# Kernel optimization log

Hardware: AMD Instinct MI355X
Metric: run time of the kernel (lower is better)

## Reference

```python
import jax, jax.numpy as jnp
import numpy as np
import math

DIM_PER_HEAD = 64

def setup_inputs() -> dict:
    key = jax.random.key(0)
    k1, k2, k3, k4 = jax.random.split(key, 4)
    B, H, S, D = 2, 16, 2048, 64
    mat1 = jax.random.normal(k1, (B, H, S, D), dtype=jnp.float32)
    mat2 = jax.random.normal(k2, (B, H, S, D), dtype=jnp.float32)
    mat3 = jax.random.normal(k3, (B, H, S, D), dtype=jnp.float32)
    bias = jax.random.normal(k4, (1, 1, S, S), dtype=jnp.float32)
    return {"mat1": mat1, "mat2": mat2, "mat3": mat3, "bias": bias}

def reference(mat1, mat2, mat3, bias) -> jnp.ndarray:
    # scale Q, scores = QK^T + bias, softmax over last dim, then @ V
    scale = 1.0 / math.sqrt(DIM_PER_HEAD)
    qk = jnp.einsum('bhqd,bhkd->bhqk', mat1 * scale, mat2)  # [B,H,S,S]
    scores = jax.nn.softmax(qk + bias, axis=-1)
    return jnp.einsum('bhqk,bhkd->bhqd', scores, mat3)
```

## Files before the change

### kernel.cpp

```cpp
#include <hip/hip_runtime.h>
#include <hip/hip_bf16.h>


#define SEQ 2048
#define DH  64
#define BHN 32
#define LOG2E 1.44269504088896f

typedef __attribute__((ext_vector_type(8))) short bf16x8;
typedef __attribute__((ext_vector_type(4))) float f32x4;
typedef __attribute__((ext_vector_type(8))) short short8v;

__device__ inline short f2b(float x) {
    union { float f; unsigned u; } v; v.f = x;
    unsigned r = v.u + 0x7fff + ((v.u >> 16) & 1);
    return (short)(r >> 16);
}

__device__ inline void gl_lds16(const void* g, void* l) {
    __builtin_amdgcn_global_load_lds(
        (const __attribute__((address_space(1))) void*)g,
        (__attribute__((address_space(3))) void*)l, 16, 0, 0);
}

__global__ __launch_bounds__(256)
void prep_kv(const float* __restrict__ K, const float* __restrict__ V,
             short* __restrict__ Kb, short* __restrict__ Vt) {
    __shared__ short t[64 * 72];
    const int tid = threadIdx.x;
    const int bh = blockIdx.x >> 5, st = blockIdx.x & 31, s0 = st * 64;

    {
        const float* Kp = K + ((size_t)bh * SEQ + s0) * DH;
        short* Ko = Kb + ((size_t)bh * SEQ + s0) * DH;
        #pragma unroll
        for (int i = 0; i < 2; ++i) {
            size_t o = (size_t)(tid + i * 256) * 8;
            f32x4 a = *(const f32x4*)(Kp + o);
            f32x4 b = *(const f32x4*)(Kp + o + 4);
            short8v s;
            #pragma unroll
            for (int j = 0; j < 4; ++j) { s[j] = f2b(a[j]); s[4 + j] = f2b(b[j]); }
            *(short8v*)(Ko + o) = s;
        }
    }

    const float* Vb = V + (size_t)bh * SEQ * DH + (size_t)s0 * DH;
    #pragma unroll
    for (int i = 0; i < 4; ++i) {
        int c = tid + i * 256, s = c >> 4, c4 = c & 15;
        f32x4 v = *(const f32x4*)(Vb + s * DH + c4 * 4);
        #pragma unroll
        for (int j = 0; j < 4; ++j) t[s * 72 + c4 * 4 + j] = f2b(v[j]);
    }
    __syncthreads();
    const int d = tid >> 2, part = tid & 3;
    short8v lo, hi;
    #pragma unroll
    for (int j = 0; j < 8; ++j) {
        lo[j] = t[(part * 16 + j) * 72 + d];
        hi[j] = t[(part * 16 + 8 + j) * 72 + d];
    }
    short* outp = Vt + (size_t)bh * DH * SEQ + (size_t)d * SEQ + s0 + part * 16;
    *(short8v*)outp = lo;
    *(short8v*)(outp + 8) = hi;
}

__global__ __launch_bounds__(256, 4)
void mha_main(const float* __restrict__ Q, const float* __restrict__ Bias,
              const short* __restrict__ Kb, const short* __restrict__ Vt,
              float* __restrict__ Out)
{
    __shared__ short ka[64 * DH];
    __shared__ short kbuf[64 * DH];
    __shared__ short va[64 * DH];
    __shared__ short vbuf[64 * DH];
    __shared__ short lds_p[4 * 16 * 64];

    const int tid = threadIdx.x, lane = tid & 63, wave = tid >> 6;
    const int l15 = lane & 15, l4 = lane >> 4;
    const int qb = blockIdx.x & 31, bh = blockIdx.x >> 5;
    const int q0 = qb * 64;

    const float* Qb = Q + (size_t)bh * SEQ * DH;
    const short* Kh = Kb + (size_t)bh * SEQ * DH;
    const short* Vh = Vt + (size_t)bh * DH * SEQ;
    float* Ob = Out + (size_t)bh * SEQ * DH;

    bf16x8 qf[2];
    {
        const float* qp = Qb + (size_t)(q0 + wave * 16 + l15) * DH;
        #pragma unroll
        for (int ks = 0; ks < 2; ++ks) {
            short tmp[8];
            #pragma unroll
            for (int j = 0; j < 8; ++j) tmp[j] = f2b(qp[ks * 32 + l4 * 8 + j] * 0.125f);
            qf[ks] = *reinterpret_cast<bf16x8*>(tmp);
        }
    }

    f32x4 o_acc[4];
    #pragma unroll
    for (int dt = 0; dt < 4; ++dt) o_acc[dt] = f32x4{0.f, 0.f, 0.f, 0.f};
    float l_part[4] = {0.f, 0.f, 0.f, 0.f};

    const short *kg0, *kg1, *vg0, *vg1;
    int off0, off1;
    {
        int s0_ = wave * 64 + lane, r0 = s0_ >> 3, c0 = s0_ & 7, g0 = c0 ^ (r0 & 7);
        int s1_ = 256 + wave * 64 + lane, r1 = s1_ >> 3, c1 = s1_ & 7, g1 = c1 ^ (r1 & 7);
        kg0 = Kh + (size_t)r0 * DH + g0 * 8;
        vg0 = Vh + (size_t)r0 * SEQ + g0 * 8;
        kg1 = Kh + (size_t)r1 * DH + g1 * 8;
        vg1 = Vh + (size_t)r1 * SEQ + g1 * 8;
        off0 = (wave * 64) * 8;
        off1 = (256 + wave * 64) * 8;
    }
    const float* bp0 = Bias + (size_t)(q0 + wave * 16 + l4 * 4) * SEQ + l15;
    short* pw = &lds_p[wave * 16 * 64];
    const int swz = l15 & 7;

    gl_lds16(kg0, ka + off0);
    gl_lds16(kg1, ka + off1);
    gl_lds16(vg0, va + off0);
    gl_lds16(vg1, va + off1);

    auto tile = [&](int kt, const short* kc, const short* vc,
                    short* knx, short* vnx) {
        const float* bp = bp0 + kt * 64;
        float bv[4][4];
        #pragma unroll
        for (int r = 0; r < 4; ++r)
            #pragma unroll
            for (int nt = 0; nt < 4; ++nt)
                bv[r][nt] = bp[(size_t)r * SEQ + nt * 16];

        const int kn = (kt + 1) & 31;
        gl_lds16(kg0 + (size_t)kn * 64 * DH, knx + off0);
        gl_lds16(kg1 + (size_t)kn * 64 * DH, knx + off1);
        gl_lds16(vg0 + kn * 64, vnx + off0);
        gl_lds16(vg1 + kn * 64, vnx + off1);

        asm volatile("s_waitcnt vmcnt(20)\n\ts_barrier" ::: "memory");

        f32x4 sacc[4];
        #pragma unroll
        for (int nt = 0; nt < 4; ++nt) sacc[nt] = f32x4{0.f, 0.f, 0.f, 0.f};
        #pragma unroll
        for (int ks = 0; ks < 2; ++ks)
            #pragma unroll
            for (int nt = 0; nt < 4; ++nt) {
                int cc = (ks * 4 + l4) ^ swz;
                bf16x8 kf = *(const bf16x8*)&kc[(nt * 16 + l15) * DH + cc * 8];
                sacc[nt] = __builtin_amdgcn_mfma_f32_16x16x32_bf16(qf[ks], kf, sacc[nt], 0, 0, 0);
            }

        #pragma unroll
        for (int r = 0; r < 4; ++r) {
            const int prow = l4 * 4 + r;
            const int rsw = prow & 7;
            #pragma unroll
            for (int nt = 0; nt < 4; ++nt) {
                float pv = __builtin_amdgcn_exp2f((sacc[nt][r] + bv[r][nt]) * LOG2E);
                l_part[r] += pv;
                int pc = (nt * 2 + (l15 >> 3)) ^ rsw;
                pw[prow * 64 + pc * 8 + (l15 & 7)] = f2b(pv);
            }
        }

        #pragma unroll
        for (int ks = 0; ks < 2; ++ks) {
            int cc = (ks * 4 + l4) ^ swz;
            bf16x8 pf = *(const bf16x8*)&pw[l15 * 64 + cc * 8];
            #pragma unroll
            for (int dt = 0; dt < 4; ++dt) {
                bf16x8 vf = *(const bf16x8*)&vc[(dt * 16 + l15) * DH + cc * 8];
                o_acc[dt] = __builtin_amdgcn_mfma_f32_16x16x32_bf16(pf, vf, o_acc[dt], 0, 0, 0);
            }
        }

        asm volatile("s_barrier" ::: "memory");
    };

    for (int kt = 0; kt < SEQ / 64; kt += 2) {
        tile(kt,     ka,   va,   kbuf, vbuf);
        tile(kt + 1, kbuf, vbuf, ka,   va);
    }

    #pragma unroll
    for (int r = 0; r < 4; ++r) {
        float s = l_part[r];
        #pragma unroll
        for (int m = 1; m < 16; m <<= 1) s += __shfl_xor(s, m, 64);
        l_part[r] = s;
    }

    #pragma unroll
    for (int r = 0; r < 4; ++r) {
        float inv = 1.0f / l_part[r];
        float* op = Ob + (size_t)(q0 + wave * 16 + l4 * 4 + r) * DH + l15;
        #pragma unroll
        for (int dt = 0; dt < 4; ++dt) op[dt * 16] = o_acc[dt][r] * inv;
    }
}

extern "C" void kernel_launch(void* const* d_in, const int* in_sizes, int n_in,
                              void* d_out, int out_size, void* d_ws, size_t ws_size,
                              hipStream_t stream) {
    const float* Q    = (const float*)d_in[0];
    const float* K    = (const float*)d_in[1];
    const float* V    = (const float*)d_in[2];
    const float* Bias = (const float*)d_in[3];
    float* O          = (float*)d_out;

    short* Kb = (short*)d_ws;
    short* Vt = Kb + (size_t)BHN * SEQ * DH;

    prep_kv<<<dim3(BHN * 32), dim3(256), 0, stream>>>(K, V, Kb, Vt);
    mha_main<<<dim3(BHN * 32), dim3(256), 0, stream>>>(Q, Bias, Kb, Vt, O);
}
```

Before: 169.5 us.

## Keep softmax probabilities in registers by transposing QK^T and permuting V rows

Swaps the operand order of the score MFMA so each lane holds a key-column slice of the scores. That lets the exponentiated probabilities be packed directly into the A-operand of the PV MFMA, removing the LDS write/read round trip for P. To match the register-layout permutation, prep_kv now writes the transposed V with a row permutation. Other changes: LOG2E is folded into the Q scale, bias is loaded as contiguous float4 per lane, the row-sum reduction is simplified, and the vmcnt wait threshold is tightened. A wrong permutation would silently corrupt results.

```diff
diff --git a/kernel.cpp b/kernel.cpp
--- a/kernel.cpp
+++ b/kernel.cpp
@@ -21,6 +21,10 @@
     __builtin_amdgcn_global_load_lds(
         (const __attribute__((address_space(1))) void*)g,
         (__attribute__((address_space(3))) void*)l, 16, 0, 0);
+}
+
+__device__ __host__ inline int phi(int r) {
+    return 32 * (r >> 5) + 16 * ((r >> 2) & 1) + 4 * ((r >> 3) & 3) + (r & 3);
 }
 
 __global__ __launch_bounds__(256)
@@ -55,15 +59,17 @@
     }
     __syncthreads();
     const int d = tid >> 2, part = tid & 3;
-    short8v lo, hi;
-    #pragma unroll
-    for (int j = 0; j < 8; ++j) {
-        lo[j] = t[(part * 16 + j) * 72 + d];
-        hi[j] = t[(part * 16 + 8 + j) * 72 + d];
-    }
     short* outp = Vt + (size_t)bh * DH * SEQ + (size_t)d * SEQ + s0 + part * 16;
-    *(short8v*)outp = lo;
-    *(short8v*)(outp + 8) = hi;
+    #pragma unroll
+    for (int h = 0; h < 2; ++h) {
+        short8v w;
+        #pragma unroll
+        for (int u = 0; u < 8; ++u) {
+            int rho = part * 16 + h * 8 + u;
+            w[u] = t[phi(rho) * 72 + d];
+        }
+        *(short8v*)(outp + h * 8) = w;
+    }
 }
 
 __global__ __launch_bounds__(256, 4)
@@ -75,7 +81,6 @@
     __shared__ short kbuf[64 * DH];
     __shared__ short va[64 * DH];
     __shared__ short vbuf[64 * DH];
-    __shared__ short lds_p[4 * 16 * 64];
 
     const int tid = threadIdx.x, lane = tid & 63, wave = tid >> 6;
     const int l15 = lane & 15, l4 = lane >> 4;
@@ -94,7 +99,7 @@
         for (int ks = 0; ks < 2; ++ks) {
             short tmp[8];
             #pragma unroll
-            for (int j = 0; j < 8; ++j) tmp[j] = f2b(qp[ks * 32 + l4 * 8 + j] * 0.125f);
+            for (int j = 0; j < 8; ++j) tmp[j] = f2b(qp[ks * 32 + l4 * 8 + j] * (0.125f * LOG2E));
             qf[ks] = *reinterpret_cast<bf16x8*>(tmp);
         }
     }
@@ -102,7 +107,7 @@
     f32x4 o_acc[4];
     #pragma unroll
     for (int dt = 0; dt < 4; ++dt) o_acc[dt] = f32x4{0.f, 0.f, 0.f, 0.f};
-    float l_part[4] = {0.f, 0.f, 0.f, 0.f};
+    float l_part = 0.f;
 
     const short *kg0, *kg1, *vg0, *vg1;
     int off0, off1;
@@ -116,8 +121,7 @@
         off0 = (wave * 64) * 8;
         off1 = (256 + wave * 64) * 8;
     }
-    const float* bp0 = Bias + (size_t)(q0 + wave * 16 + l4 * 4) * SEQ + l15;
-    short* pw = &lds_p[wave * 16 * 64];
+    const float* bp0 = Bias + (size_t)(q0 + wave * 16 + l15) * SEQ + l4 * 4;
     const int swz = l15 & 7;
 
     gl_lds16(kg0, ka + off0);
@@ -127,13 +131,11 @@
 
     auto tile = [&](int kt, const short* kc, const short* vc,
                     short* knx, short* vnx) {
+        f32x4 bv[4];
         const float* bp = bp0 + kt * 64;
-        float bv[4][4];
-        #pragma unroll
-        for (int r = 0; r < 4; ++r)
-            #pragma unroll
-            for (int nt = 0; nt < 4; ++nt)
-                bv[r][nt] = bp[(size_t)r * SEQ + nt * 16];
+        #pragma unroll
+        for (int nt = 0; nt < 4; ++nt)
+            bv[nt] = *(const f32x4*)(bp + nt * 16);
 
         const int kn = (kt + 1) & 31;
         gl_lds16(kg0 + (size_t)kn * 64 * DH, knx + off0);
@@ -141,7 +143,7 @@
         gl_lds16(vg0 + kn * 64, vnx + off0);
         gl_lds16(vg1 + kn * 64, vnx + off1);
 
-        asm volatile("s_waitcnt vmcnt(20)\n\ts_barrier" ::: "memory");
+        asm volatile("s_waitcnt vmcnt(8)\n\ts_barrier" ::: "memory");
 
         f32x4 sacc[4];
         #pragma unroll
@@ -152,30 +154,35 @@
             for (int nt = 0; nt < 4; ++nt) {
                 int cc = (ks * 4 + l4) ^ swz;
                 bf16x8 kf = *(const bf16x8*)&kc[(nt * 16 + l15) * DH + cc * 8];
-                sacc[nt] = __builtin_amdgcn_mfma_f32_16x16x32_bf16(qf[ks], kf, sacc[nt], 0, 0, 0);
-            }
-
-        #pragma unroll
-        for (int r = 0; r < 4; ++r) {
-            const int prow = l4 * 4 + r;
-            const int rsw = prow & 7;
-            #pragma unroll
-            for (int nt = 0; nt < 4; ++nt) {
-                float pv = __builtin_amdgcn_exp2f((sacc[nt][r] + bv[r][nt]) * LOG2E);
-                l_part[r] += pv;
-                int pc = (nt * 2 + (l15 >> 3)) ^ rsw;
-                pw[prow * 64 + pc * 8 + (l15 & 7)] = f2b(pv);
+                sacc[nt] = __builtin_amdgcn_mfma_f32_16x16x32_bf16(kf, qf[ks], sacc[nt], 0, 0, 0);
+            }
+
+        unsigned pk[4][2];
+        #pragma unroll
+        for (int nt = 0; nt < 4; ++nt) {
+            float pv[4];
+            #pragma unroll
+            for (int r = 0; r < 4; ++r) {
+                pv[r] = __builtin_amdgcn_exp2f(__builtin_fmaf(bv[nt][r], LOG2E, sacc[nt][r]));
+                l_part += pv[r];
+            }
+            #pragma unroll
+            for (int rp = 0; rp < 2; ++rp) {
+                __hip_bfloat162 h2 = __float22bfloat162_rn(float2{pv[2 * rp], pv[2 * rp + 1]});
+                pk[nt][rp] = *reinterpret_cast<unsigned*>(&h2);
             }
         }
 
         #pragma unroll
         for (int ks = 0; ks < 2; ++ks) {
-            int cc = (ks * 4 + l4) ^ swz;
-            bf16x8 pf = *(const bf16x8*)&pw[l15 * 64 + cc * 8];
+            union { bf16x8 v; unsigned u[4]; } af;
+            af.u[0] = pk[2 * ks][0]; af.u[1] = pk[2 * ks][1];
+            af.u[2] = pk[2 * ks + 1][0]; af.u[3] = pk[2 * ks + 1][1];
             #pragma unroll
             for (int dt = 0; dt < 4; ++dt) {
+                int cc = (ks * 4 + l4) ^ swz;
                 bf16x8 vf = *(const bf16x8*)&vc[(dt * 16 + l15) * DH + cc * 8];
-                o_acc[dt] = __builtin_amdgcn_mfma_f32_16x16x32_bf16(pf, vf, o_acc[dt], 0, 0, 0);
+                o_acc[dt] = __builtin_amdgcn_mfma_f32_16x16x32_bf16(af.v, vf, o_acc[dt], 0, 0, 0);
             }
         }
 
@@ -187,17 +194,13 @@
         tile(kt + 1, kbuf, vbuf, ka,   va);
     }
 
+    l_part += __shfl_xor(l_part, 16, 64);
+    l_part += __shfl_xor(l_part, 32, 64);
+
     #pragma unroll
     for (int r = 0; r < 4; ++r) {
-        float s = l_part[r];
-        #pragma unroll
-        for (int m = 1; m < 16; m <<= 1) s += __shfl_xor(s, m, 64);
-        l_part[r] = s;
-    }
-
-    #pragma unroll
-    for (int r = 0; r < 4; ++r) {
-        float inv = 1.0f / l_part[r];
+        float lr = __shfl(l_part, l4 * 4 + r, 64);
+        float inv = 1.0f / lr;
         float* op = Ob + (size_t)(q0 + wave * 16 + l4 * 4 + r) * DH + l15;
         #pragma unroll
         for (int dt = 0; dt < 4; ++dt) op[dt * 16] = o_acc[dt][r] * inv;
```

Result: slower. 184.1 us (+8.6%).
